# Performance work log

Measured on AMD Instinct MI355X. Metric: run time of the kernel, lower is better.

## Reference

```python
import jax, jax.numpy as jnp
import numpy as np

B, TP, TF, C, H, W = 8, 3, 4, 256, 64, 64
BN_EPS = 1e-3  # YOLOX BaseConv BatchNorm2d eps


def setup_inputs() -> dict:
    key = jax.random.key(0)
    ks = jax.random.split(key, 12)
    s = 1.0 / np.sqrt(C)
    return {
        "feature": jax.random.normal(ks[0], (B, TP + 1, C, H, W), jnp.float32),
        "past_time_constant": jax.random.normal(ks[1], (B, TP), jnp.float32),
        "future_time_constant": jax.random.normal(ks[2], (B, TF), jnp.float32),
        # fc_time_constant: Linear(1, C)
        "w_tc": jax.random.normal(ks[3], (C, 1), jnp.float32),
        "b_tc": jax.random.normal(ks[4], (C,), jnp.float32) * 0.1,
        # fc_in: Linear(2C, C)
        "w_in": jax.random.normal(ks[5], (C, 2 * C), jnp.float32) * (1.0 / np.sqrt(2 * C)),
        "b_in": jnp.zeros((C,), jnp.float32),
        # conv_p: 1x1 conv (no bias) + BN + SiLU
        "conv_w": jax.random.normal(ks[6], (C, C), jnp.float32) * s,
        "bn_gamma": jnp.ones((C,), jnp.float32),
        "bn_beta": jnp.zeros((C,), jnp.float32),
        "bn_mean": jax.random.normal(ks[7], (C,), jnp.float32) * 0.1,
        "bn_var": jnp.ones((C,), jnp.float32) + jax.random.uniform(ks[8], (C,)) * 0.1,
        # fc_query / fc_key: Linear(C, C)
        "w_q": jax.random.normal(ks[9], (C, C), jnp.float32) * s,
        "b_q": jnp.zeros((C,), jnp.float32),
        "w_k": jax.random.normal(ks[10], (C, C), jnp.float32) * s,
        "b_k": jnp.zeros((C,), jnp.float32),
        # p_attn: [1,1,C,1,1]
        "p_attn": jnp.ones((1, 1, C, 1, 1), jnp.float32),
    }


def reference(feature, past_time_constant, future_time_constant,
              w_tc, b_tc, w_in, b_in, conv_w, bn_gamma, bn_beta, bn_mean, bn_var,
              w_q, b_q, w_k, b_k, p_attn):
    b, t1, c, h, w = feature.shape
    tp = past_time_constant.shape[1]
    tf = future_time_constant.shape[1]
    silu = jax.nn.silu

    # conv_p = 1x1 conv (bias=False) + BatchNorm(eval) + SiLU, over all TP+1 frames
    x = jnp.einsum('oc,btchw->btohw', conv_w, feature)
    scale = bn_gamma / jnp.sqrt(bn_var + BN_EPS)          # [C]
    x = x * scale[:, None, None] + (bn_beta - bn_mean * scale)[:, None, None]
    feature_p = silu(x)                                    # [B,TP+1,C,H,W]

    # time-constant embeddings: tanh(Linear(1->C))
    ptc = jnp.tanh(past_time_constant[..., None] * w_tc[:, 0] + b_tc)    # [B,TP,C]
    ftc = jnp.tanh(future_time_constant[..., None] * w_tc[:, 0] + b_tc)  # [B,TF,C]

    # past branch: global max+avg pool over HxW, concat, fc_in+SiLU, add ptc
    fp_past = feature_p[:, :-1]                            # [B,TP,C,H,W]
    pool_p = jnp.concatenate([fp_past.max(axis=(-2, -1)), fp_past.mean(axis=(-2, -1))], axis=-1)  # [B,TP,2C]
    attn_in_p = silu(jnp.einsum('oc,btc->bto', w_in, pool_p) + b_in) + ptc  # [B,TP,C]

    # future branch: feature_f = last raw frame broadcast over TF (pool identical per TF)
    last = feature[:, -1]                                  # [B,C,H,W]
    pool_f = jnp.concatenate([last.max(axis=(-2, -1)), last.mean(axis=(-2, -1))], axis=-1)  # [B,2C]
    attn_in_f = silu(pool_f @ w_in.T + b_in)[:, None, :] + ftc  # [B,TF,C]

    q = attn_in_f @ w_q.T + b_q                            # [B,TF,C]
    k = attn_in_p @ w_k.T + b_k                            # [B,TP,C]
    v = (feature_p[:, -1:] - fp_past).reshape(b, tp, c * h * w)  # [B,TP,CHW]

    # NOTE: torch code scales by sqrt(attn_query.size(1)) == sqrt(TF), not sqrt(C)
    attn_w = jnp.einsum('bfc,bpc->bfp', q, k) / jnp.sqrt(jnp.asarray(tf, q.dtype))  # [B,TF,TP]
    attn = jnp.einsum('bfp,bpd->bfd', attn_w, v).reshape(b, tf, c, h, w)

    # residual: feature_f + attn * p_attn / attn_key.size(1) (== TP)
    out = last[:, None] + attn * p_attn / tp               # [B,TF,C,H,W]
    return out
```

## Files before the change

### kernel.cpp

```cpp
#include <hip/hip_runtime.h>

#define B_   8
#define T1_  4
#define TP_  3
#define TF_  4
#define C_   256
#define HW_  4096

#define OFF_FP     0ull
#define OFF_PMAXK  67108864ull
#define OFF_PSUM   67133440ull
#define OFF_RMAX   67158016ull
#define OFF_RSUM   67166208ull
#define OFF_Q      67174400ull
#define OFF_K      67207168ull
#define OFF_AW     67231744ull
#define OFF_WFRAG  67232128ull
#define WS_NEED    67363200ull

typedef __attribute__((ext_vector_type(8))) short bf16x8;
typedef __attribute__((ext_vector_type(4))) float f32x4;

__device__ __forceinline__ unsigned short f2bf(float f) {
    unsigned int u = __float_as_uint(f);
    u += 0x7fffu + ((u >> 16) & 1u);
    return (unsigned short)(u >> 16);
}
__device__ __forceinline__ unsigned int cvtpk(float lo, float hi) {
    unsigned int r;
    asm("v_cvt_pk_bf16_f32 %0, %1, %2" : "=v"(r) : "v"(lo), "v"(hi));
    return r;
}
__device__ __forceinline__ unsigned int fkey(float x) {
    unsigned int b = __float_as_uint(x);
    return (b & 0x80000000u) ? ~b : (b | 0x80000000u);
}
__device__ __forceinline__ float funkey(unsigned int k) {
    unsigned int b = (k & 0x80000000u) ? (k ^ 0x80000000u) : ~k;
    return __uint_as_float(b);
}
__device__ __forceinline__ float silu_f(float x) { return x / (1.0f + __expf(-x)); }

__device__ __forceinline__ void dec8(uint4 u, float* f) {
    f[0] = __uint_as_float(u.x << 16); f[1] = __uint_as_float(u.x & 0xffff0000u);
    f[2] = __uint_as_float(u.y << 16); f[3] = __uint_as_float(u.y & 0xffff0000u);
    f[4] = __uint_as_float(u.z << 16); f[5] = __uint_as_float(u.z & 0xffff0000u);
    f[6] = __uint_as_float(u.w << 16); f[7] = __uint_as_float(u.w & 0xffff0000u);
}

__global__ __launch_bounds__(256) void k_wpre(const float* __restrict__ Wc,
                                              unsigned short* __restrict__ wfrag) {
    const int idx = blockIdx.x * 256 + threadIdx.x;
    const int j   = idx & 7;
    const int fi  = idx >> 3;
    const int col = fi & 15;
    const int q   = (fi >> 4) & 3;
    const int sob = fi >> 6;
    const int ob  = sob & 15;
    const int s   = sob >> 4;
    const int o   = ob * 16 + col;
    const int c   = s * 32 + q * 8 + j;
    wfrag[idx] = f2bf(Wc[o * 256 + c]);
}

__global__ __launch_bounds__(256) void k0_rawpool(const float* __restrict__ feature,
                                                  float* __restrict__ rmax,
                                                  float* __restrict__ rsum) {
    const int blk = blockIdx.x;
    const int b = blk >> 8, c = blk & 255;
    const float* base = feature + ((size_t)(b * 4 + 3) * C_ + c) * HW_;
    const int tid = threadIdx.x;
    float mx = -3.4e38f, sm = 0.0f;
    #pragma unroll
    for (int k = 0; k < 4; ++k) {
        float4 v = *(const float4*)(base + (k * 256 + tid) * 4);
        mx = fmaxf(mx, fmaxf(fmaxf(v.x, v.y), fmaxf(v.z, v.w)));
        sm += (v.x + v.y) + (v.z + v.w);
    }
    #pragma unroll
    for (int m = 1; m < 64; m <<= 1) {
        mx = fmaxf(mx, __shfl_xor(mx, m));
        sm += __shfl_xor(sm, m);
    }
    __shared__ float wmx[4], wsm[4];
    const int wave = tid >> 6;
    if ((tid & 63) == 0) { wmx[wave] = mx; wsm[wave] = sm; }
    __syncthreads();
    if (tid == 0) {
        rmax[b * C_ + c] = fmaxf(fmaxf(wmx[0], wmx[1]), fmaxf(wmx[2], wmx[3]));
        rsum[b * C_ + c] = (wsm[0] + wsm[1]) + (wsm[2] + wsm[3]);
    }
}

__global__ __launch_bounds__(256) void k1_conv(
    const float* __restrict__ feature, const unsigned short* __restrict__ wfrag,
    const float* __restrict__ gamma, const float* __restrict__ beta,
    const float* __restrict__ mean, const float* __restrict__ var,
    unsigned short* __restrict__ fp_out,
    unsigned int* __restrict__ pmaxk, float* __restrict__ psum) {
    __shared__ __align__(16) unsigned short lds_b[64 * 40];
    __shared__ float s_scale[256];
    __shared__ float s_shift[256];

    const int tid   = threadIdx.x;
    const int bt    = blockIdx.x >> 6;
    const int hwblk = blockIdx.x & 63;
    const int b = bt >> 2, t = bt & 3;
    const int hw0 = hwblk * 64;
    const int lane = tid & 63;
    const int wave = tid >> 6;
    const int q = lane >> 4;
    const int col = lane & 15;
    const int hwl = tid & 63;

    {
        float sc = gamma[tid] * rsqrtf(var[tid] + 1e-3f);
        s_scale[tid] = sc;
        s_shift[tid] = beta[tid] - mean[tid] * sc;
    }

    const float* Fb = feature + (size_t)bt * C_ * HW_;
    f32x4 acc[4][4] = {};

    float fv[8];
    #pragma unroll
    for (int j = 0; j < 8; ++j)
        fv[j] = Fb[(size_t)(wave * 8 + j) * HW_ + hw0 + hwl];
    bf16x8 afr[4];
    #pragma unroll
    for (int mi = 0; mi < 4; ++mi)
        afr[mi] = *(const bf16x8*)(wfrag + ((size_t)(wave * 4 + mi) * 64 + lane) * 8);

    #pragma unroll
    for (int s = 0; s < 8; ++s) {
        __syncthreads();
        uint4 pk;
        pk.x = cvtpk(fv[0], fv[1]);
        pk.y = cvtpk(fv[2], fv[3]);
        pk.z = cvtpk(fv[4], fv[5]);
        pk.w = cvtpk(fv[6], fv[7]);
        *(uint4*)&lds_b[hwl * 40 + wave * 8] = pk;
        __syncthreads();

        bf16x8 bfr[4];
        #pragma unroll
        for (int ni = 0; ni < 4; ++ni)
            bfr[ni] = *(const bf16x8*)&lds_b[(ni * 16 + col) * 40 + q * 8];

        bf16x8 afn[4];
        if (s < 7) {
            #pragma unroll
            for (int j = 0; j < 8; ++j)
                fv[j] = Fb[(size_t)((s + 1) * 32 + wave * 8 + j) * HW_ + hw0 + hwl];
            #pragma unroll
            for (int mi = 0; mi < 4; ++mi)
                afn[mi] = *(const bf16x8*)(wfrag +
                           ((size_t)((s + 1) * 16 + wave * 4 + mi) * 64 + lane) * 8);
        }

        #pragma unroll
        for (int mi = 0; mi < 4; ++mi)
            #pragma unroll
            for (int ni = 0; ni < 4; ++ni)
                acc[mi][ni] = __builtin_amdgcn_mfma_f32_16x16x32_bf16(
                    afr[mi], bfr[ni], acc[mi][ni], 0, 0, 0);

        if (s < 7) {
            #pragma unroll
            for (int mi = 0; mi < 4; ++mi) afr[mi] = afn[mi];
        }
    }

    unsigned short* fpo = fp_out + (size_t)bt * C_ * HW_;
    #pragma unroll
    for (int mi = 0; mi < 4; ++mi) {
        #pragma unroll
        for (int r = 0; r < 4; ++r) {
            const int o = wave * 64 + mi * 16 + q * 4 + r;
            const float sc = s_scale[o], sh = s_shift[o];
            float mx = -3.4e38f, sm = 0.0f;
            #pragma unroll
            for (int ni = 0; ni < 4; ++ni) {
                float x = acc[mi][ni][r] * sc + sh;
                float sl = silu_f(x);
                fpo[(size_t)o * HW_ + hw0 + ni * 16 + col] = f2bf(sl);
                mx = fmaxf(mx, sl);
                sm += sl;
            }
            if (t < 3) {
                #pragma unroll
                for (int m = 1; m < 16; m <<= 1) {
                    mx = fmaxf(mx, __shfl_xor(mx, m));
                    sm += __shfl_xor(sm, m);
                }
                if (col == 0) {
                    atomicMax(&pmaxk[(b * 3 + t) * C_ + o], fkey(mx));
                    atomicAdd(&psum[(b * 3 + t) * C_ + o], sm);
                }
            }
        }
    }
}

__global__ __launch_bounds__(256) void k2_vec(
    const float* __restrict__ past_tc, const float* __restrict__ fut_tc,
    const float* __restrict__ w_tc, const float* __restrict__ b_tc,
    const float* __restrict__ w_in, const float* __restrict__ b_in,
    const float* __restrict__ w_q, const float* __restrict__ b_q,
    const float* __restrict__ w_k, const float* __restrict__ b_k,
    const unsigned int* __restrict__ pmaxk, const float* __restrict__ psum,
    const float* __restrict__ rmax, const float* __restrict__ rsum,
    float* __restrict__ qout, float* __restrict__ kout) {
    __shared__ float pool[512];
    __shared__ float avec[256];
    const int b = blockIdx.x / 7;
    const int idx = blockIdx.x % 7;
    const int o = threadIdx.x;
    const bool pside = (idx < 3);
    if (pside) {
        pool[o]       = funkey(pmaxk[(b * 3 + idx) * C_ + o]);
        pool[256 + o] = psum[(b * 3 + idx) * C_ + o] * (1.0f / 4096.0f);
    } else {
        pool[o]       = rmax[b * C_ + o];
        pool[256 + o] = rsum[b * C_ + o] * (1.0f / 4096.0f);
    }
    __syncthreads();
    float s = b_in[o];
    const float* wr = w_in + (size_t)o * 512;
    #pragma unroll 8
    for (int c = 0; c < 512; ++c) s += wr[c] * pool[c];
    float v = silu_f(s);
    float tcin = pside ? past_tc[b * 3 + idx] : fut_tc[b * 4 + (idx - 3)];
    float tc = tanhf(tcin * w_tc[o] + b_tc[o]);
    avec[o] = v + tc;
    __syncthreads();
    if (pside) {
        float s2 = b_k[o];
        const float* wk = w_k + (size_t)o * 256;
        #pragma unroll 8
        for (int c = 0; c < 256; ++c) s2 += wk[c] * avec[c];
        kout[(b * 3 + idx) * C_ + o] = s2;
    } else {
        float s2 = b_q[o];
        const float* wq = w_q + (size_t)o * 256;
        #pragma unroll 8
        for (int c = 0; c < 256; ++c) s2 += wq[c] * avec[c];
        qout[(b * 4 + (idx - 3)) * C_ + o] = s2;
    }
}

__global__ __launch_bounds__(64) void k2_attnw(const float* __restrict__ qv,
                                               const float* __restrict__ kv,
                                               float* __restrict__ aw) {
    const int i = blockIdx.x;
    const int b = i / 12, rr = i % 12, f = rr / 3, p = rr % 3;
    const int lane = threadIdx.x;
    const float* qp = qv + (b * 4 + f) * C_;
    const float* kp = kv + (b * 3 + p) * C_;
    float s = 0.0f;
    #pragma unroll
    for (int j = 0; j < 4; ++j) s += qp[lane + 64 * j] * kp[lane + 64 * j];
    #pragma unroll
    for (int m = 1; m < 64; m <<= 1) s += __shfl_xor(s, m);
    if (lane == 0) aw[b * 12 + rr] = s * 0.5f;
}

__global__ __launch_bounds__(256) void k3_out(
    const float* __restrict__ feature, const unsigned short* __restrict__ fp,
    const float* __restrict__ aw, const float* __restrict__ p_attn,
    float* __restrict__ out) {
    const int idx = blockIdx.x;
    const int b = idx >> 9;
    const int c = (idx >> 1) & 255;
    const int half = idx & 1;
    const int hw = half * 2048 + threadIdx.x * 8;

    float a[12];
    #pragma unroll
    for (int i = 0; i < 12; ++i) a[i] = aw[b * 12 + i];
    const float pa = p_attn[c] * (1.0f / 3.0f);

    const size_t ts = (size_t)C_ * HW_;
    const size_t base = ((size_t)(b * 4) * C_ + c) * HW_ + hw;

    uint4 u0 = *(const uint4*)(fp + base);
    uint4 u1 = *(const uint4*)(fp + base + ts);
    uint4 u2 = *(const uint4*)(fp + base + 2 * ts);
    uint4 u3 = *(const uint4*)(fp + base + 3 * ts);
    float4 l0 = *(const float4*)(feature + base + 3 * ts);
    float4 l1 = *(const float4*)(feature + base + 3 * ts + 4);

    float f0[8], f1[8], f2[8], f3[8];
    dec8(u0, f0); dec8(u1, f1); dec8(u2, f2); dec8(u3, f3);
    float lastv[8] = {l0.x, l0.y, l0.z, l0.w, l1.x, l1.y, l1.z, l1.w};

    float ov[4][8];
    #pragma unroll
    for (int e = 0; e < 8; ++e) {
        float d0 = f3[e] - f0[e];
        float d1 = f3[e] - f1[e];
        float d2 = f3[e] - f2[e];
        #pragma unroll
        for (int f = 0; f < 4; ++f) {
            float at = a[f * 3 + 0] * d0 + a[f * 3 + 1] * d1 + a[f * 3 + 2] * d2;
            ov[f][e] = lastv[e] + at * pa;
        }
    }
    #pragma unroll
    for (int f = 0; f < 4; ++f) {
        size_t ob = ((size_t)(b * 4 + f) * C_ + c) * HW_ + hw;
        *(float4*)(out + ob)     = make_float4(ov[f][0], ov[f][1], ov[f][2], ov[f][3]);
        *(float4*)(out + ob + 4) = make_float4(ov[f][4], ov[f][5], ov[f][6], ov[f][7]);
    }
}

extern "C" void kernel_launch(void* const* d_in, const int* in_sizes, int n_in,
                              void* d_out, int out_size, void* d_ws, size_t ws_size,
                              hipStream_t stream) {
    const float* feature = (const float*)d_in[0];
    const float* past_tc = (const float*)d_in[1];
    const float* fut_tc  = (const float*)d_in[2];
    const float* w_tc    = (const float*)d_in[3];
    const float* b_tc    = (const float*)d_in[4];
    const float* w_in    = (const float*)d_in[5];
    const float* b_in    = (const float*)d_in[6];
    const float* conv_w  = (const float*)d_in[7];
    const float* gamma   = (const float*)d_in[8];
    const float* beta    = (const float*)d_in[9];
    const float* mean    = (const float*)d_in[10];
    const float* var     = (const float*)d_in[11];
    const float* w_q     = (const float*)d_in[12];
    const float* b_q     = (const float*)d_in[13];
    const float* w_k     = (const float*)d_in[14];
    const float* b_k     = (const float*)d_in[15];
    const float* p_attn  = (const float*)d_in[16];

    char* ws = (char*)d_ws;
    unsigned short* fp  = (unsigned short*)(ws + OFF_FP);
    unsigned int* pmaxk = (unsigned int*)(ws + OFF_PMAXK);
    float* psum = (float*)(ws + OFF_PSUM);
    float* rmax = (float*)(ws + OFF_RMAX);
    float* rsum = (float*)(ws + OFF_RSUM);
    float* qout = (float*)(ws + OFF_Q);
    float* kout = (float*)(ws + OFF_K);
    float* aw   = (float*)(ws + OFF_AW);
    unsigned short* wfrag = (ws_size >= WS_NEED)
        ? (unsigned short*)(ws + OFF_WFRAG)
        : (unsigned short*)((char*)d_out + (size_t)out_size - 131072);

    hipMemsetAsync(ws + OFF_PMAXK, 0, 49152, stream);

    k_wpre<<<256, 256, 0, stream>>>(conv_w, wfrag);
    k0_rawpool<<<B_ * C_, 256, 0, stream>>>(feature, rmax, rsum);
    k1_conv<<<B_ * T1_ * 64, 256, 0, stream>>>(feature, wfrag, gamma, beta, mean, var,
                                               fp, pmaxk, psum);
    k2_vec<<<B_ * 7, 256, 0, stream>>>(past_tc, fut_tc, w_tc, b_tc, w_in, b_in,
                                       w_q, b_q, w_k, b_k, pmaxk, psum, rmax, rsum,
                                       qout, kout);
    k2_attnw<<<B_ * TF_ * TP_, 64, 0, stream>>>(qout, kout, aw);
    k3_out<<<B_ * C_ * 2, 256, 0, stream>>>(feature, fp, aw, p_attn, (float*)d_out);
}
```

Measured before the change: 350.7 us.

## Load conv B-fragments directly from global, drop LDS staging and barriers

The 1x1 conv kernel no longer stages feature tiles through shared memory. Each wave now loads its own MFMA B-fragments straight from global memory and converts them to bf16 in registers, which removes the per-step LDS writes and the two barriers. The cost is that all four waves load the same feature tile, so global/L2 traffic for features rises about fourfold, and the explicit software prefetch of the next step is gone. A launch-bounds occupancy hint of 2 is also added.

```diff
diff --git a/kernel.cpp b/kernel.cpp
--- a/kernel.cpp
+++ b/kernel.cpp
@@ -92,13 +92,12 @@
     }
 }
 
-__global__ __launch_bounds__(256) void k1_conv(
+__global__ __launch_bounds__(256, 2) void k1_conv(
     const float* __restrict__ feature, const unsigned short* __restrict__ wfrag,
     const float* __restrict__ gamma, const float* __restrict__ beta,
     const float* __restrict__ mean, const float* __restrict__ var,
     unsigned short* __restrict__ fp_out,
     unsigned int* __restrict__ pmaxk, float* __restrict__ psum) {
-    __shared__ __align__(16) unsigned short lds_b[64 * 40];
     __shared__ float s_scale[256];
     __shared__ float s_shift[256];
 
@@ -111,51 +110,40 @@
     const int wave = tid >> 6;
     const int q = lane >> 4;
     const int col = lane & 15;
-    const int hwl = tid & 63;
 
     {
         float sc = gamma[tid] * rsqrtf(var[tid] + 1e-3f);
         s_scale[tid] = sc;
         s_shift[tid] = beta[tid] - mean[tid] * sc;
     }
-
-    const float* Fb = feature + (size_t)bt * C_ * HW_;
+    __syncthreads();
+
+    const float* Fq = feature + (size_t)bt * C_ * HW_ + (size_t)(q * 8) * HW_
+                      + hw0 + col;
+    const unsigned short* Wq = wfrag + ((size_t)(wave * 4) * 64 + lane) * 8;
+
     f32x4 acc[4][4] = {};
 
-    float fv[8];
-    #pragma unroll
-    for (int j = 0; j < 8; ++j)
-        fv[j] = Fb[(size_t)(wave * 8 + j) * HW_ + hw0 + hwl];
-    bf16x8 afr[4];
-    #pragma unroll
-    for (int mi = 0; mi < 4; ++mi)
-        afr[mi] = *(const bf16x8*)(wfrag + ((size_t)(wave * 4 + mi) * 64 + lane) * 8);
-
     #pragma unroll
     for (int s = 0; s < 8; ++s) {
-        __syncthreads();
-        uint4 pk;
-        pk.x = cvtpk(fv[0], fv[1]);
-        pk.y = cvtpk(fv[2], fv[3]);
-        pk.z = cvtpk(fv[4], fv[5]);
-        pk.w = cvtpk(fv[6], fv[7]);
-        *(uint4*)&lds_b[hwl * 40 + wave * 8] = pk;
-        __syncthreads();
+        bf16x8 afr[4];
+        #pragma unroll
+        for (int mi = 0; mi < 4; ++mi)
+            afr[mi] = *(const bf16x8*)(Wq + (size_t)((s * 16 + mi) * 64) * 8);
 
         bf16x8 bfr[4];
         #pragma unroll
-        for (int ni = 0; ni < 4; ++ni)
-            bfr[ni] = *(const bf16x8*)&lds_b[(ni * 16 + col) * 40 + q * 8];
-
-        bf16x8 afn[4];
-        if (s < 7) {
+        for (int ni = 0; ni < 4; ++ni) {
+            float fv[8];
             #pragma unroll
             for (int j = 0; j < 8; ++j)
-                fv[j] = Fb[(size_t)((s + 1) * 32 + wave * 8 + j) * HW_ + hw0 + hwl];
-            #pragma unroll
-            for (int mi = 0; mi < 4; ++mi)
-                afn[mi] = *(const bf16x8*)(wfrag +
-                           ((size_t)((s + 1) * 16 + wave * 4 + mi) * 64 + lane) * 8);
+                fv[j] = Fq[(size_t)(s * 32 + j) * HW_ + ni * 16];
+            uint4 pk;
+            pk.x = cvtpk(fv[0], fv[1]);
+            pk.y = cvtpk(fv[2], fv[3]);
+            pk.z = cvtpk(fv[4], fv[5]);
+            pk.w = cvtpk(fv[6], fv[7]);
+            bfr[ni] = __builtin_bit_cast(bf16x8, pk);
         }
 
         #pragma unroll
@@ -164,11 +152,6 @@
             for (int ni = 0; ni < 4; ++ni)
                 acc[mi][ni] = __builtin_amdgcn_mfma_f32_16x16x32_bf16(
                     afr[mi], bfr[ni], acc[mi][ni], 0, 0, 0);
-
-        if (s < 7) {
-            #pragma unroll
-            for (int mi = 0; mi < 4; ++mi) afr[mi] = afn[mi];
-        }
     }
 
     unsigned short* fpo = fp_out + (size_t)bt * C_ * HW_;
```

New measurement: 368.7 us. 5.1% more time.
